# Optimization experiments

Hardware: AMD Instinct MI355X
Metric: run time of the kernel (lower is better)

## Reference

```python
import jax, jax.numpy as jnp
import numpy as np

F_THRESHOLD = 10  # zero out DCT coefficients with i + j <= 10 (low-frequency triangle)


def _dct_mat(N):
    # torch_dct.dct with norm=None: X_k = 2 * sum_n x_n cos(pi*(2n+1)*k/(2N))
    n = np.arange(N)
    k = np.arange(N)[:, None]
    return (2.0 * np.cos(np.pi * (2 * n + 1) * k / (2 * N))).astype(np.float32)  # [k, n]


def _idct_mat(N):
    # inverse of the norm=None DCT-II above: x_n = (1/N) * sum_k w_k X_k cos(pi*(2n+1)*k/(2N)), w_0=0.5
    n = np.arange(N)[:, None]
    k = np.arange(N)
    w = np.ones(N, dtype=np.float64)
    w[0] = 0.5
    return ((w * np.cos(np.pi * (2 * n + 1) * k / (2 * N))) / N).astype(np.float32)  # [n, k]


def _filtermask(H, W):
    i = jnp.arange(H)[:, None]
    j = jnp.arange(W)[None, :]
    return jnp.where(i + j <= F_THRESHOLD, 0.0, 1.0).astype(jnp.float32)  # [H, W]


def setup_inputs() -> dict:
    key = jax.random.key(0)
    im = jax.random.normal(key, (32, 3, 512, 512), dtype=jnp.float32)
    return {"im": im}


def reference(im) -> jnp.ndarray:
    B, C, H, W = im.shape
    Ch = jnp.asarray(_dct_mat(H))   # [kh, h]
    Cw = jnp.asarray(_dct_mat(W))   # [kw, w]
    Dh = jnp.asarray(_idct_mat(H))  # [h, kh]
    Dw = jnp.asarray(_idct_mat(W))  # [w, kw]
    mask = _filtermask(H, W)

    # dct_2d: DCT-II along W then along H
    x = jnp.einsum('kh,bchw,lw->bckl', Ch, im, Cw)
    x = x * mask  # zero low-frequency triangle
    # idct_2d
    x = jnp.einsum('hk,bckl,wl->bchw', Dh, x, Dw)
    return x
```

## Files before the change

kernel.cpp:

```cpp
#include <hip/hip_runtime.h>
#include <math.h>

#define NPIX 512
#define NK 11
#define NPAIR 121
#define RBLKS 8
#define NCH 96

#define PI_D 3.14159265358979323846

__global__ void build_C(float* __restrict__ Ct) {
    int k = blockIdx.x;
    int h = threadIdx.x;
    double v = 2.0 * cos(PI_D * (double)((2 * h + 1) * k) / 1024.0);
    Ct[k * NPIX + h] = (float)v;
}

#define AS_LD 516
__global__ __launch_bounds__(256) void k_partial(const float* __restrict__ im,
                                                 const float* __restrict__ Ct,
                                                 float* __restrict__ plow) {
    __shared__ float Cs[NK][NPIX];
    __shared__ float As[NK][AS_LD];

    int bid = blockIdx.x;
    int c = bid >> 3, rb = bid & 7;
    int t = threadIdx.x;

    for (int i = t; i < NK * NPIX; i += 256) ((float*)Cs)[i] = Ct[i];
    __syncthreads();

    int half = t >> 7;
    int col4 = t & 127;
    int w0 = col4 * 4;
    int rowbase = rb * 64 + half * 32;
    const float* imc = im + (size_t)c * NPIX * NPIX;

    float a[NK][4];
#pragma unroll
    for (int k = 0; k < NK; ++k)
        for (int j = 0; j < 4; ++j) a[k][j] = 0.f;

    for (int i = 0; i < 32; ++i) {
        int h = rowbase + i;
        float4 v = *(const float4*)(imc + (size_t)h * NPIX + w0);
#pragma unroll
        for (int k = 0; k < NK; ++k) {
            float ch = Cs[k][h];
            a[k][0] += ch * v.x;
            a[k][1] += ch * v.y;
            a[k][2] += ch * v.z;
            a[k][3] += ch * v.w;
        }
    }

    if (half == 0) {
#pragma unroll
        for (int k = 0; k < NK; ++k)
            *(float4*)&As[k][w0] = make_float4(a[k][0], a[k][1], a[k][2], a[k][3]);
    }
    __syncthreads();
    if (half == 1) {
#pragma unroll
        for (int k = 0; k < NK; ++k) {
            float4 cur = *(float4*)&As[k][w0];
            cur.x += a[k][0]; cur.y += a[k][1]; cur.z += a[k][2]; cur.w += a[k][3];
            *(float4*)&As[k][w0] = cur;
        }
    }
    __syncthreads();

    int k = t >> 4;
    int sub = t & 15;
    if (k < NK) {
        float* outp = plow + (size_t)bid * NPAIR + k * NK;
        for (int l = 0; l < NK; ++l) {
            float acc = 0.f;
#pragma unroll
            for (int wi = 0; wi < 32; ++wi) {
                int w = wi * 16 + sub;
                acc += As[k][w] * Cs[l][w];
            }
            acc += __shfl_xor(acc, 8);
            acc += __shfl_xor(acc, 4);
            acc += __shfl_xor(acc, 2);
            acc += __shfl_xor(acc, 1);
            if (sub == 0) outp[l] = acc;
        }
    }
}

__global__ void k_final(const float* __restrict__ plow, float* __restrict__ lows) {
    int c = blockIdx.x;
    int t = threadIdx.x;
    if (t >= NPAIR) return;
    int k = t / NK, l = t % NK;
    float s = 0.f;
    for (int b = 0; b < RBLKS; ++b) s += plow[((size_t)c * RBLKS + b) * NPAIR + t];
    float sk = (k == 0 ? 0.5f : 1.0f) * (1.0f / 1024.0f);
    float sl = (l == 0 ? 0.5f : 1.0f) * (1.0f / 1024.0f);
    lows[(size_t)c * NPAIR + t] = (k + l <= 10) ? s * sk * sl : 0.f;
}

__global__ __launch_bounds__(256) void k_output(const float* __restrict__ im,
                                                const float* __restrict__ Ct,
                                                const float* __restrict__ lows,
                                                float* __restrict__ out) {
    __shared__ float Cs[NK][NPIX];
    __shared__ float Ls[NPAIR];

    int bid = blockIdx.x;
    int c = bid >> 3, rb = bid & 7;
    int t = threadIdx.x;

    for (int i = t; i < NK * NPIX; i += 256) ((float*)Cs)[i] = Ct[i];
    if (t < NPAIR) Ls[t] = lows[(size_t)c * NPAIR + t];
    __syncthreads();

    int half = t >> 7;
    int col4 = t & 127;
    int w0 = col4 * 4;
    int rowbase = rb * 64 + half * 32;

    float B[NK][4];
#pragma unroll
    for (int k = 0; k < NK; ++k)
        for (int j = 0; j < 4; ++j) B[k][j] = 0.f;

#pragma unroll
    for (int l = 0; l < NK; ++l) {
        float4 cl = *(const float4*)&Cs[l][w0];
#pragma unroll
        for (int k = 0; k < NK; ++k) {
            float lw = Ls[k * NK + l];
            B[k][0] += lw * cl.x;
            B[k][1] += lw * cl.y;
            B[k][2] += lw * cl.z;
            B[k][3] += lw * cl.w;
        }
    }

    const float* imc = im + (size_t)c * NPIX * NPIX;
    float* outc = out + (size_t)c * NPIX * NPIX;

    for (int i = 0; i < 32; ++i) {
        int h = rowbase + i;
        float4 v = *(const float4*)(imc + (size_t)h * NPIX + w0);
        float c0 = 0.f, c1 = 0.f, c2 = 0.f, c3 = 0.f;
#pragma unroll
        for (int k = 0; k < NK; ++k) {
            float ch = Cs[k][h];
            c0 += ch * B[k][0];
            c1 += ch * B[k][1];
            c2 += ch * B[k][2];
            c3 += ch * B[k][3];
        }
        float4 o = make_float4(v.x - c0, v.y - c1, v.z - c2, v.w - c3);
        *(float4*)(outc + (size_t)h * NPIX + w0) = o;
    }
}

extern "C" void kernel_launch(void* const* d_in, const int* in_sizes, int n_in,
                              void* d_out, int out_size, void* d_ws, size_t ws_size,
                              hipStream_t stream) {
    const float* im = (const float*)d_in[0];
    float* out = (float*)d_out;

    float* ws = (float*)d_ws;
    float* Ct = ws;
    float* plow = Ct + NK * NPIX;
    float* lows = plow + (size_t)NCH * RBLKS * NPAIR;

    build_C<<<NK, NPIX, 0, stream>>>(Ct);
    k_partial<<<NCH * RBLKS, 256, 0, stream>>>(im, Ct, plow);
    k_final<<<NCH, 128, 0, stream>>>(plow, lows);
    k_output<<<NCH * RBLKS, 256, 0, stream>>>(im, Ct, lows, out);
}
```

Baseline: 72.10 us.

## Fuse cosine table build and final reduction into main kernels, drop two launches

The standalone cosine-table kernel is removed. Each block now computes the 11x512 DCT cosine table directly into shared memory using float cosf with exact integer phase reduction. The per-channel reduction and masking kernel is folded into the start of the output kernel. This cuts the pipeline from four launches to two, trading launch overhead and global round trips for redundant per-block cosf work and slightly lower-precision table values.

```diff
diff --git a/kernel.cpp b/kernel.cpp
--- a/kernel.cpp
+++ b/kernel.cpp
@@ -7,18 +7,21 @@
 #define RBLKS 8
 #define NCH 96
 
-#define PI_D 3.14159265358979323846
+#define PI_F 3.14159265358979323846f
 
-__global__ void build_C(float* __restrict__ Ct) {
-    int k = blockIdx.x;
-    int h = threadIdx.x;
-    double v = 2.0 * cos(PI_D * (double)((2 * h + 1) * k) / 1024.0);
-    Ct[k * NPIX + h] = (float)v;
+__device__ inline void build_Cs(float (*Cs)[NPIX], int t) {
+#pragma unroll
+    for (int i = t; i < NK * NPIX; i += 256) {
+        int k = i >> 9;
+        int h = i & 511;
+        int m = ((2 * h + 1) * k) & 2047;
+        float ang = (float)m * (PI_F / 1024.0f);
+        ((float*)Cs)[i] = 2.0f * cosf(ang);
+    }
 }
 
 #define AS_LD 516
 __global__ __launch_bounds__(256) void k_partial(const float* __restrict__ im,
-                                                 const float* __restrict__ Ct,
                                                  float* __restrict__ plow) {
     __shared__ float Cs[NK][NPIX];
     __shared__ float As[NK][AS_LD];
@@ -27,7 +30,7 @@
     int c = bid >> 3, rb = bid & 7;
     int t = threadIdx.x;
 
-    for (int i = t; i < NK * NPIX; i += 256) ((float*)Cs)[i] = Ct[i];
+    build_Cs(Cs, t);
     __syncthreads();
 
     int half = t >> 7;
@@ -90,21 +93,8 @@
     }
 }
 
-__global__ void k_final(const float* __restrict__ plow, float* __restrict__ lows) {
-    int c = blockIdx.x;
-    int t = threadIdx.x;
-    if (t >= NPAIR) return;
-    int k = t / NK, l = t % NK;
-    float s = 0.f;
-    for (int b = 0; b < RBLKS; ++b) s += plow[((size_t)c * RBLKS + b) * NPAIR + t];
-    float sk = (k == 0 ? 0.5f : 1.0f) * (1.0f / 1024.0f);
-    float sl = (l == 0 ? 0.5f : 1.0f) * (1.0f / 1024.0f);
-    lows[(size_t)c * NPAIR + t] = (k + l <= 10) ? s * sk * sl : 0.f;
-}
-
 __global__ __launch_bounds__(256) void k_output(const float* __restrict__ im,
-                                                const float* __restrict__ Ct,
-                                                const float* __restrict__ lows,
+                                                const float* __restrict__ plow,
                                                 float* __restrict__ out) {
     __shared__ float Cs[NK][NPIX];
     __shared__ float Ls[NPAIR];
@@ -113,8 +103,18 @@
     int c = bid >> 3, rb = bid & 7;
     int t = threadIdx.x;
 
-    for (int i = t; i < NK * NPIX; i += 256) ((float*)Cs)[i] = Ct[i];
-    if (t < NPAIR) Ls[t] = lows[(size_t)c * NPAIR + t];
+    build_Cs(Cs, t);
+
+    if (t < NPAIR) {
+        int k = t / NK, l = t % NK;
+        float s = 0.f;
+        const float* pp = plow + (size_t)c * RBLKS * NPAIR + t;
+#pragma unroll
+        for (int b = 0; b < RBLKS; ++b) s += pp[b * NPAIR];
+        float sk = (k == 0 ? 0.5f : 1.0f) * (1.0f / 1024.0f);
+        float sl = (l == 0 ? 0.5f : 1.0f) * (1.0f / 1024.0f);
+        Ls[t] = (k + l <= 10) ? s * sk * sl : 0.f;
+    }
     __syncthreads();
 
     int half = t >> 7;
@@ -165,14 +165,8 @@
                               hipStream_t stream) {
     const float* im = (const float*)d_in[0];
     float* out = (float*)d_out;
+    float* plow = (float*)d_ws;
 
-    float* ws = (float*)d_ws;
-    float* Ct = ws;
-    float* plow = Ct + NK * NPIX;
-    float* lows = plow + (size_t)NCH * RBLKS * NPAIR;
-
-    build_C<<<NK, NPIX, 0, stream>>>(Ct);
-    k_partial<<<NCH * RBLKS, 256, 0, stream>>>(im, Ct, plow);
-    k_final<<<NCH, 128, 0, stream>>>(plow, lows);
-    k_output<<<NCH * RBLKS, 256, 0, stream>>>(im, Ct, lows, out);
+    k_partial<<<NCH * RBLKS, 256, 0, stream>>>(im, plow);
+    k_output<<<NCH * RBLKS, 256, 0, stream>>>(im, plow, out);
 }
```

New measurement: 67.35 us. -6.6%, faster.
